# Performance work log

Measured on AMD Instinct MI355X. Metric: run time of the kernel, lower is better.

The kernel has to match this reference:

```python
import jax, jax.numpy as jnp
import numpy as np

B, S, IN, H = 16, 512, 512, 256
TAU_TRACE = 20.0
TAU_MEM = 20.0
DECAY_TRACE = float(np.exp(-1.0 / TAU_TRACE))  # exp_convolve decay
DECAY_MEM = float(np.exp(-1.0 / TAU_MEM))      # leaky-integrator dynamics decay
LR = 0.01                                       # plasticity learning rate
W_MAX = 1.0                                     # soft upper bound on fast weights


def setup_inputs() -> dict:
    key = jax.random.key(0)
    k1, k2 = jax.random.split(key)
    x = jax.random.normal(k1, (B, S, IN), dtype=jnp.float32)
    # xavier_uniform with gain=sqrt(2) on W of shape [2H, IN]
    lim = float(np.sqrt(2.0) * np.sqrt(6.0 / (2 * H + IN)))
    W = jax.random.uniform(k2, (2 * H, IN), dtype=jnp.float32, minval=-lim, maxval=lim)
    return {"x": x, "W": W}


def reference(x, W):
    # i = x @ W^T : [B, S, 2H], then split into key/value input currents
    i = jnp.einsum('bsi,hi->bsh', x, W)
    ik, iv = jnp.split(i, 2, axis=2)  # each [B, S, H]
    bsz = x.shape[0]
    h = W.shape[0] // 2

    def step(carry, inp):
        kv, vv, kt, vt, mem = carry
        ik_t, iv_t = inp  # [B, H] each
        # key dynamics (leaky integrator + tanh)
        kv = DECAY_MEM * kv + ik_t
        key = jnp.tanh(kv)
        # memory readout: 0.2 * (key.unsqueeze(1) * mem).sum(2) == 0.2 * mem @ key
        ikv = 0.2 * jnp.einsum('bij,bj->bi', mem, key)
        # value dynamics
        vv = DECAY_MEM * vv + iv_t + ikv
        val = jnp.tanh(vv)
        # exponential traces
        kt = DECAY_TRACE * kt + (1.0 - DECAY_TRACE) * key
        vt = DECAY_TRACE * vt + (1.0 - DECAY_TRACE) * val
        # soft-bounded Hebbian outer-product fast-weight update
        mem = mem + LR * (vt[:, :, None] * kt[:, None, :]) * (W_MAX - mem)
        return (kv, vv, kt, vt, mem), (key, val)

    z = jnp.zeros((bsz, h), x.dtype)
    mem0 = jnp.zeros((bsz, h, h), x.dtype)
    (_, _, _, _, mem), (keys, vals) = jax.lax.scan(
        step, (z, z, z, z, mem0),
        (jnp.swapaxes(ik, 0, 1), jnp.swapaxes(iv, 0, 1)))  # scan over time
    return mem, jnp.swapaxes(keys, 0, 1), jnp.swapaxes(vals, 0, 1)
```

## Files before the change

### kernel.cpp

```cpp
#include <hip/hip_runtime.h>

#define BB 16
#define SS 512
#define KIN 512
#define H 256

typedef float v2f __attribute__((ext_vector_type(2)));

constexpr float DECAY = 0.951229424500714f;
constexpr float OMD   = 0.048770575499286f;
constexpr float LR    = 0.01f;

__device__ __forceinline__ float fast_tanh(float x) {
    float e = __expf(2.f * x);
    return 1.f - __fdividef(2.f, e + 1.f);
}

__device__ __forceinline__ v2f pk_mul(v2f a, v2f b) {
    v2f d; asm("v_pk_mul_f32 %0, %1, %2" : "=v"(d) : "v"(a), "v"(b)); return d;
}
__device__ __forceinline__ v2f pk_fma(v2f a, v2f b, v2f c) {
    v2f d; asm("v_pk_fma_f32 %0, %1, %2, %3" : "=v"(d) : "v"(a), "v"(b), "v"(c)); return d;
}

__device__ __forceinline__ float allred32(float x) {
    int t;
    t = __builtin_amdgcn_update_dpp(0, __float_as_int(x), 0x111, 0xf, 0xf, false);
    x += __int_as_float(t);
    t = __builtin_amdgcn_update_dpp(0, __float_as_int(x), 0x112, 0xf, 0xf, false);
    x += __int_as_float(t);
    t = __builtin_amdgcn_update_dpp(0, __float_as_int(x), 0x114, 0xf, 0xf, false);
    x += __int_as_float(t);
    t = __builtin_amdgcn_update_dpp(0, __float_as_int(x), 0x118, 0xf, 0xf, false);
    x += __int_as_float(t);
    t = __builtin_amdgcn_update_dpp(0, __float_as_int(x), 0x142, 0xa, 0xf, false);
    x += __int_as_float(t);
    return __int_as_float(__builtin_amdgcn_ds_swizzle(__float_as_int(x), 0x3E0));
}

__global__ __launch_bounds__(256) void gemm_xwT(const float* __restrict__ X,
                                                const float* __restrict__ W,
                                                float* __restrict__ ik_out,
                                                float* __restrict__ iv_t) {
    __shared__ float As[16][68];
    __shared__ float Bs[16][68];
    const int m0 = blockIdx.y * 64;
    const int n0 = blockIdx.x * 64;
    const int tid = threadIdx.x;
    const int r  = tid >> 2;
    const int cg = tid & 3;
    const int tx = tid & 15;
    const int ty = tid >> 4;
    float acc[4][4] = {};
    for (int k0 = 0; k0 < KIN; k0 += 16) {
        float4 av = *(const float4*)&X[(size_t)(m0 + r) * KIN + k0 + cg * 4];
        float4 bv = *(const float4*)&W[(size_t)(n0 + r) * KIN + k0 + cg * 4];
        __syncthreads();
        As[cg*4+0][r] = av.x; As[cg*4+1][r] = av.y; As[cg*4+2][r] = av.z; As[cg*4+3][r] = av.w;
        Bs[cg*4+0][r] = bv.x; Bs[cg*4+1][r] = bv.y; Bs[cg*4+2][r] = bv.z; Bs[cg*4+3][r] = bv.w;
        __syncthreads();
#pragma unroll
        for (int kk = 0; kk < 16; ++kk) {
            float4 a = *(const float4*)&As[kk][ty * 4];
            float4 b = *(const float4*)&Bs[kk][tx * 4];
            float ar[4] = {a.x, a.y, a.z, a.w};
            float br[4] = {b.x, b.y, b.z, b.w};
#pragma unroll
            for (int i = 0; i < 4; ++i)
#pragma unroll
                for (int j = 0; j < 4; ++j) acc[i][j] += ar[i] * br[j];
        }
    }
    if (n0 < 256) {
#pragma unroll
        for (int i = 0; i < 4; ++i) {
            float4 o = make_float4(acc[i][0], acc[i][1], acc[i][2], acc[i][3]);
            *(float4*)&ik_out[(size_t)(m0 + ty * 4 + i) * 256 + n0 + tx * 4] = o;
        }
    } else {
        const int b  = m0 >> 9;
        const int s0 = (m0 & 511) + ty * 4;
#pragma unroll
        for (int j = 0; j < 4; ++j) {
            float4 o = make_float4(acc[0][j], acc[1][j], acc[2][j], acc[3][j]);
            *(float4*)&iv_t[((size_t)b * H + (n0 - 256 + tx * 4 + j)) * SS + s0] = o;
        }
    }
}

__global__ __launch_bounds__(64) void key_scan(float* ik,
                                               float* __restrict__ keys) {
    const int idx = blockIdx.x * 64 + threadIdx.x;
    const int b   = idx >> 8;
    const int col = idx & 255;
    float* c  = ik + (size_t)b * SS * 256 + col;
    float* ko = keys + (size_t)b * SS * H + col;
    float kv = 0.f, kt = 0.f;
    constexpr int D = 32;
    float ib[D];
#pragma unroll
    for (int j = 0; j < D; ++j) ib[j] = c[(size_t)j * 256];
    for (int t = 0; t < SS; t += D) {
#pragma unroll
        for (int j = 0; j < D; ++j) {
            float v = ib[j];
            int tn = t + D + j; if (tn > SS - 1) tn = SS - 1;
            ib[j] = c[(size_t)tn * 256];
            kv = DECAY * kv + v;
            float key = fast_tanh(kv);
            kt = __builtin_fmaf(DECAY, kt, OMD * key);
            ko[(size_t)(t + j) * H] = key;
            c[(size_t)(t + j) * 256] = kt;
        }
    }
}

__global__ __launch_bounds__(256, 2) void value_scan(const float* __restrict__ keys,
                                                     const float* __restrict__ kts,
                                                     const float* __restrict__ iv_t,
                                                     float* __restrict__ mem_out,
                                                     float* __restrict__ vals) {
    const int tid  = threadIdx.x;
    const int wave = tid >> 6;
    const int lane = tid & 63;
    const int half = lane >> 5;
    const int sub  = lane & 31;
    const int b    = blockIdx.x & 15;
    const int rg   = blockIdx.x >> 4;
    const int row  = rg * 8 + wave * 2 + half;
    const int so   = sub * 8;

    const float* kp  = keys + (size_t)b * SS * H + so;
    const float* tp  = kts  + (size_t)b * SS * H + so;
    const float* ivp = iv_t + ((size_t)b * H + row) * SS;
    float* vrow = vals + (size_t)b * SS * H + row;

    const v2f ONE2 = {1.f, 1.f};
    const v2f NM12 = {-1.f, -1.f};

    v2f mem2[4] = {{0.f,0.f},{0.f,0.f},{0.f,0.f},{0.f,0.f}};
    float vv = 0.f, vt = 0.f, stash = 0.f;

    v2f kR[8][4], tR[8][4];
#pragma unroll
    for (int j = 0; j < 8; ++j)
#pragma unroll
        for (int q = 0; q < 4; ++q) {
            kR[j][q] = *(const v2f*)(kp + (size_t)j * H + q * 2);
            tR[j][q] = *(const v2f*)(tp + (size_t)j * H + q * 2);
        }
    const float* kpF = kp + 8 * H;
    const float* tpF = tp + 8 * H;

    float4 iA0 = *(const float4*)(ivp + 0);
    float4 iA1 = *(const float4*)(ivp + 4);
    float4 iB0 = *(const float4*)(ivp + 8);
    float4 iB1 = *(const float4*)(ivp + 12);
    ivp += 16;

#define VS_STEP(J, RELOAD)                                                     \
    {                                                                          \
        v2f kc0 = kR[(J)&7][0], kc1 = kR[(J)&7][1],                            \
            kc2 = kR[(J)&7][2], kc3 = kR[(J)&7][3];                            \
        v2f tc0 = tR[(J)&7][0], tc1 = tR[(J)&7][1],                            \
            tc2 = tR[(J)&7][2], tc3 = tR[(J)&7][3];                            \
        if (RELOAD) {                                                          \
            kR[(J)&7][0] = *(const v2f*)(kpF + ((J)&3) * H + 0);               \
            kR[(J)&7][1] = *(const v2f*)(kpF + ((J)&3) * H + 2);               \
            kR[(J)&7][2] = *(const v2f*)(kpF + ((J)&3) * H + 4);               \
            kR[(J)&7][3] = *(const v2f*)(kpF + ((J)&3) * H + 6);               \
            tR[(J)&7][0] = *(const v2f*)(tpF + ((J)&3) * H + 0);               \
            tR[(J)&7][1] = *(const v2f*)(tpF + ((J)&3) * H + 2);               \
            tR[(J)&7][2] = *(const v2f*)(tpF + ((J)&3) * H + 4);               \
            tR[(J)&7][3] = *(const v2f*)(tpF + ((J)&3) * H + 6);               \
        }                                                                      \
        v2f p2 = pk_mul(mem2[0], kc0);                                         \
        p2 = pk_fma(mem2[1], kc1, p2);                                         \
        p2 = pk_fma(mem2[2], kc2, p2);                                         \
        p2 = pk_fma(mem2[3], kc3, p2);                                         \
        float s = allred32(p2.x + p2.y);                                       \
        vv = __builtin_fmaf(DECAY, vv, ivs[J]);                                \
        vv = __builtin_fmaf(0.2f, s, vv);                                      \
        float valv = fast_tanh(vv);                                            \
        vt = __builtin_fmaf(DECAY, vt, OMD * valv);                            \
        if (sub == (J)) stash = valv;                                          \
        float c = LR * vt;                                                     \
        v2f c2 = {c, c};                                                       \
        v2f d0 = pk_fma(mem2[0], NM12, ONE2);                                  \
        v2f d1 = pk_fma(mem2[1], NM12, ONE2);                                  \
        v2f d2 = pk_fma(mem2[2], NM12, ONE2);                                  \
        v2f d3 = pk_fma(mem2[3], NM12, ONE2);                                  \
        mem2[0] = pk_fma(pk_mul(c2, tc0), d0, mem2[0]);                        \
        mem2[1] = pk_fma(pk_mul(c2, tc1), d1, mem2[1]);                        \
        mem2[2] = pk_fma(pk_mul(c2, tc2), d2, mem2[2]);                        \
        mem2[3] = pk_fma(pk_mul(c2, tc3), d3, mem2[3]);                        \
        asm volatile("" ::: "memory");                                         \
    }

    for (int t0 = 0; t0 < SS - 16; t0 += 16) {
        float4 nA0 = *(const float4*)(ivp + 0);
        float4 nA1 = *(const float4*)(ivp + 4);
        float4 nB0 = *(const float4*)(ivp + 8);
        float4 nB1 = *(const float4*)(ivp + 12);
        ivp += 16;
        {
            float ivs[16] = {iA0.x, iA0.y, iA0.z, iA0.w,
                             iA1.x, iA1.y, iA1.z, iA1.w,
                             iB0.x, iB0.y, iB0.z, iB0.w,
                             iB1.x, iB1.y, iB1.z, iB1.w};
            VS_STEP(0, 1)  VS_STEP(1, 1)  VS_STEP(2, 1)  VS_STEP(3, 1)
            kpF += 4 * H; tpF += 4 * H;
            VS_STEP(4, 1)  VS_STEP(5, 1)  VS_STEP(6, 1)  VS_STEP(7, 1)
            kpF += 4 * H; tpF += 4 * H;
            VS_STEP(8, 1)  VS_STEP(9, 1)  VS_STEP(10, 1) VS_STEP(11, 1)
            kpF += 4 * H; tpF += 4 * H;
            VS_STEP(12, 1) VS_STEP(13, 1) VS_STEP(14, 1) VS_STEP(15, 1)
            kpF += 4 * H; tpF += 4 * H;
        }
        if (sub < 16) vrow[(size_t)sub * H] = stash;
        vrow += 16 * H;
        iA0 = nA0; iA1 = nA1; iB0 = nB0; iB1 = nB1;
    }
    {
        float ivs[16] = {iA0.x, iA0.y, iA0.z, iA0.w,
                         iA1.x, iA1.y, iA1.z, iA1.w,
                         iB0.x, iB0.y, iB0.z, iB0.w,
                         iB1.x, iB1.y, iB1.z, iB1.w};
        VS_STEP(0, 1)  VS_STEP(1, 1)  VS_STEP(2, 1)  VS_STEP(3, 1)
        kpF += 4 * H; tpF += 4 * H;
        VS_STEP(4, 1)  VS_STEP(5, 1)  VS_STEP(6, 1)  VS_STEP(7, 1)
        VS_STEP(8, 0)  VS_STEP(9, 0)  VS_STEP(10, 0) VS_STEP(11, 0)
        VS_STEP(12, 0) VS_STEP(13, 0) VS_STEP(14, 0) VS_STEP(15, 0)
        if (sub < 16) vrow[(size_t)sub * H] = stash;
    }
#undef VS_STEP

    float* mo = &mem_out[((size_t)b * H + row) * H + so];
    *(float4*)&mo[0] = make_float4(mem2[0].x, mem2[0].y, mem2[1].x, mem2[1].y);
    *(float4*)&mo[4] = make_float4(mem2[2].x, mem2[2].y, mem2[3].x, mem2[3].y);
}

extern "C" void kernel_launch(void* const* d_in, const int* in_sizes, int n_in,
                              void* d_out, int out_size, void* d_ws, size_t ws_size,
                              hipStream_t stream) {
    const float* x = (const float*)d_in[0];
    const float* W = (const float*)d_in[1];
    float* out = (float*)d_out;
    float* mem_out = out;
    float* keys = out + (size_t)BB * H * H;
    float* vals = keys + (size_t)BB * SS * H;
    float* ik   = (float*)d_ws;
    float* iv_t = ik + (size_t)BB * SS * 256;

    dim3 gb(8, 128);
    gemm_xwT<<<gb, 256, 0, stream>>>(x, W, ik, iv_t);
    key_scan<<<64, 64, 0, stream>>>(ik, keys);
    value_scan<<<512, 256, 0, stream>>>(keys, ik, iv_t, mem_out, vals);
}
```

Baseline: 266.7 us.

## Reformulate fast-weight update to take tanh-dependent reductions off the serial critical path

Rewrites the per-step memory update algebraically. The state is kept as negated memory plus a precomputed weight vector w = t*(1-mem), and the readout for step t+1 is split into two dot products: one against the already-updated memory and one against w, scaled by the next learning coefficient. Both cross-lane reductions can then be issued before the tanh of the current step finishes, which shortens the serial dependency chain per timestep. In exchange each step does an extra dot product and an extra all-reduce, keys are loaded one step ahead, and float rounding differs slightly from the direct update.

```diff
diff --git a/kernel.cpp b/kernel.cpp
--- a/kernel.cpp
+++ b/kernel.cpp
@@ -123,8 +123,8 @@
     const int tid  = threadIdx.x;
     const int wave = tid >> 6;
     const int lane = tid & 63;
+    const int sub  = lane & 31;
     const int half = lane >> 5;
-    const int sub  = lane & 31;
     const int b    = blockIdx.x & 15;
     const int rg   = blockIdx.x >> 4;
     const int row  = rg * 8 + wave * 2 + half;
@@ -135,21 +135,19 @@
     const float* ivp = iv_t + ((size_t)b * H + row) * SS;
     float* vrow = vals + (size_t)b * SS * H + row;
 
-    const v2f ONE2 = {1.f, 1.f};
-    const v2f NM12 = {-1.f, -1.f};
-
-    v2f mem2[4] = {{0.f,0.f},{0.f,0.f},{0.f,0.f},{0.f,0.f}};
-    float vv = 0.f, vt = 0.f, stash = 0.f;
+    v2f nm0 = {0.f,0.f}, nm1 = {0.f,0.f}, nm2 = {0.f,0.f}, nm3 = {0.f,0.f};
+    v2f w0  = {0.f,0.f}, w1  = {0.f,0.f}, w2  = {0.f,0.f}, w3  = {0.f,0.f};
+    float vv = 0.f, vt = 0.f, c = 0.f, ar = 0.f, br = 0.f, stash = 0.f;
 
     v2f kR[8][4], tR[8][4];
 #pragma unroll
     for (int j = 0; j < 8; ++j)
 #pragma unroll
         for (int q = 0; q < 4; ++q) {
-            kR[j][q] = *(const v2f*)(kp + (size_t)j * H + q * 2);
+            kR[j][q] = *(const v2f*)(kp + (size_t)(1 + j) * H + q * 2);
             tR[j][q] = *(const v2f*)(tp + (size_t)j * H + q * 2);
         }
-    const float* kpF = kp + 8 * H;
+    const float* kpF = kp + 9 * H;
     const float* tpF = tp + 8 * H;
 
     float4 iA0 = *(const float4*)(ivp + 0);
@@ -158,42 +156,52 @@
     float4 iB1 = *(const float4*)(ivp + 12);
     ivp += 16;
 
-#define VS_STEP(J, RELOAD)                                                     \
+#define VS_STEP(J, RELK, RELT)                                                 \
     {                                                                          \
         v2f kc0 = kR[(J)&7][0], kc1 = kR[(J)&7][1],                            \
             kc2 = kR[(J)&7][2], kc3 = kR[(J)&7][3];                            \
         v2f tc0 = tR[(J)&7][0], tc1 = tR[(J)&7][1],                            \
             tc2 = tR[(J)&7][2], tc3 = tR[(J)&7][3];                            \
-        if (RELOAD) {                                                          \
+        if (RELK) {                                                            \
             kR[(J)&7][0] = *(const v2f*)(kpF + ((J)&3) * H + 0);               \
             kR[(J)&7][1] = *(const v2f*)(kpF + ((J)&3) * H + 2);               \
             kR[(J)&7][2] = *(const v2f*)(kpF + ((J)&3) * H + 4);               \
             kR[(J)&7][3] = *(const v2f*)(kpF + ((J)&3) * H + 6);               \
+        }                                                                      \
+        if (RELT) {                                                            \
             tR[(J)&7][0] = *(const v2f*)(tpF + ((J)&3) * H + 0);               \
             tR[(J)&7][1] = *(const v2f*)(tpF + ((J)&3) * H + 2);               \
             tR[(J)&7][2] = *(const v2f*)(tpF + ((J)&3) * H + 4);               \
             tR[(J)&7][3] = *(const v2f*)(tpF + ((J)&3) * H + 6);               \
         }                                                                      \
-        v2f p2 = pk_mul(mem2[0], kc0);                                         \
-        p2 = pk_fma(mem2[1], kc1, p2);                                         \
-        p2 = pk_fma(mem2[2], kc2, p2);                                         \
-        p2 = pk_fma(mem2[3], kc3, p2);                                         \
-        float s = allred32(p2.x + p2.y);                                       \
-        vv = __builtin_fmaf(DECAY, vv, ivs[J]);                                \
-        vv = __builtin_fmaf(0.2f, s, vv);                                      \
+                                   \
+        v2f nc2 = {-c, -c};                                                    \
+        nm0 = pk_fma(nc2, w0, nm0);                                            \
+        nm1 = pk_fma(nc2, w1, nm1);                                            \
+        nm2 = pk_fma(nc2, w2, nm2);                                            \
+        nm3 = pk_fma(nc2, w3, nm3);                       \
+        v2f a2 = pk_mul(nm0, kc0);                                             \
+        a2 = pk_fma(nm1, kc1, a2);                                             \
+        a2 = pk_fma(nm2, kc2, a2);                                             \
+        a2 = pk_fma(nm3, kc3, a2);                    \
+        w0 = pk_fma(tc0, nm0, tc0);                                            \
+        w1 = pk_fma(tc1, nm1, tc1);                                            \
+        w2 = pk_fma(tc2, nm2, tc2);                                            \
+        w3 = pk_fma(tc3, nm3, tc3);               \
+        v2f b2 = pk_mul(w0, kc0);                                              \
+        b2 = pk_fma(w1, kc1, b2);                                              \
+        b2 = pk_fma(w2, kc2, b2);                                              \
+        b2 = pk_fma(w3, kc3, b2);                      \
+        float arn = -0.2f * allred32(a2.x + a2.y);                             \
+        float brn =  0.2f * allred32(b2.x + b2.y);                             \
+                  \
+        float vvt = __builtin_fmaf(DECAY, vv, ivs[J]) + ar;                    \
+        vv = __builtin_fmaf(c, br, vvt);                                       \
         float valv = fast_tanh(vv);                                            \
         vt = __builtin_fmaf(DECAY, vt, OMD * valv);                            \
         if (sub == (J)) stash = valv;                                          \
-        float c = LR * vt;                                                     \
-        v2f c2 = {c, c};                                                       \
-        v2f d0 = pk_fma(mem2[0], NM12, ONE2);                                  \
-        v2f d1 = pk_fma(mem2[1], NM12, ONE2);                                  \
-        v2f d2 = pk_fma(mem2[2], NM12, ONE2);                                  \
-        v2f d3 = pk_fma(mem2[3], NM12, ONE2);                                  \
-        mem2[0] = pk_fma(pk_mul(c2, tc0), d0, mem2[0]);                        \
-        mem2[1] = pk_fma(pk_mul(c2, tc1), d1, mem2[1]);                        \
-        mem2[2] = pk_fma(pk_mul(c2, tc2), d2, mem2[2]);                        \
-        mem2[3] = pk_fma(pk_mul(c2, tc3), d3, mem2[3]);                        \
+        c = LR * vt;                                                           \
+        ar = arn; br = brn;                                                    \
         asm volatile("" ::: "memory");                                         \
     }
 
@@ -208,13 +216,13 @@
                              iA1.x, iA1.y, iA1.z, iA1.w,
                              iB0.x, iB0.y, iB0.z, iB0.w,
                              iB1.x, iB1.y, iB1.z, iB1.w};
-            VS_STEP(0, 1)  VS_STEP(1, 1)  VS_STEP(2, 1)  VS_STEP(3, 1)
-            kpF += 4 * H; tpF += 4 * H;
-            VS_STEP(4, 1)  VS_STEP(5, 1)  VS_STEP(6, 1)  VS_STEP(7, 1)
-            kpF += 4 * H; tpF += 4 * H;
-            VS_STEP(8, 1)  VS_STEP(9, 1)  VS_STEP(10, 1) VS_STEP(11, 1)
-            kpF += 4 * H; tpF += 4 * H;
-            VS_STEP(12, 1) VS_STEP(13, 1) VS_STEP(14, 1) VS_STEP(15, 1)
+            VS_STEP(0, 1, 1)  VS_STEP(1, 1, 1)  VS_STEP(2, 1, 1)  VS_STEP(3, 1, 1)
+            kpF += 4 * H; tpF += 4 * H;
+            VS_STEP(4, 1, 1)  VS_STEP(5, 1, 1)  VS_STEP(6, 1, 1)  VS_STEP(7, 1, 1)
+            kpF += 4 * H; tpF += 4 * H;
+            VS_STEP(8, 1, 1)  VS_STEP(9, 1, 1)  VS_STEP(10, 1, 1) VS_STEP(11, 1, 1)
+            kpF += 4 * H; tpF += 4 * H;
+            VS_STEP(12, 1, 1) VS_STEP(13, 1, 1) VS_STEP(14, 1, 1) VS_STEP(15, 1, 1)
             kpF += 4 * H; tpF += 4 * H;
         }
         if (sub < 16) vrow[(size_t)sub * H] = stash;
@@ -226,18 +234,25 @@
                          iA1.x, iA1.y, iA1.z, iA1.w,
                          iB0.x, iB0.y, iB0.z, iB0.w,
                          iB1.x, iB1.y, iB1.z, iB1.w};
-        VS_STEP(0, 1)  VS_STEP(1, 1)  VS_STEP(2, 1)  VS_STEP(3, 1)
+        VS_STEP(0, 1, 1)  VS_STEP(1, 1, 1)  VS_STEP(2, 1, 1)  VS_STEP(3, 1, 1)
         kpF += 4 * H; tpF += 4 * H;
-        VS_STEP(4, 1)  VS_STEP(5, 1)  VS_STEP(6, 1)  VS_STEP(7, 1)
-        VS_STEP(8, 0)  VS_STEP(9, 0)  VS_STEP(10, 0) VS_STEP(11, 0)
-        VS_STEP(12, 0) VS_STEP(13, 0) VS_STEP(14, 0) VS_STEP(15, 0)
+        VS_STEP(4, 1, 1)  VS_STEP(5, 1, 1)  VS_STEP(6, 1, 1)  VS_STEP(7, 0, 1)
+        VS_STEP(8, 0, 0)  VS_STEP(9, 0, 0)  VS_STEP(10, 0, 0) VS_STEP(11, 0, 0)
+        VS_STEP(12, 0, 0) VS_STEP(13, 0, 0) VS_STEP(14, 0, 0) VS_STEP(15, 0, 0)
         if (sub < 16) vrow[(size_t)sub * H] = stash;
     }
 #undef VS_STEP
 
+    {
+        v2f ncf = {-c, -c};
+        nm0 = pk_fma(ncf, w0, nm0);
+        nm1 = pk_fma(ncf, w1, nm1);
+        nm2 = pk_fma(ncf, w2, nm2);
+        nm3 = pk_fma(ncf, w3, nm3);
+    }
     float* mo = &mem_out[((size_t)b * H + row) * H + so];
-    *(float4*)&mo[0] = make_float4(mem2[0].x, mem2[0].y, mem2[1].x, mem2[1].y);
-    *(float4*)&mo[4] = make_float4(mem2[2].x, mem2[2].y, mem2[3].x, mem2[3].y);
+    *(float4*)&mo[0] = make_float4(-nm0.x, -nm0.y, -nm1.x, -nm1.y);
+    *(float4*)&mo[4] = make_float4(-nm2.x, -nm2.y, -nm3.x, -nm3.y);
 }
 
 extern "C" void kernel_launch(void* const* d_in, const int* in_sizes, int n_in,
```

New measurement: 334.0 us. +25.2%, slower.
